# Kernel tuning notes

Measured on AMD Instinct MI355X. Metric: run time of the kernel, lower is better.

The kernel has to match this reference:

```python
import jax, jax.numpy as jnp
import numpy as np

K = 20          # neighbors
M = 8           # weight-bank size per layer
EPS = 1e-5      # BatchNorm eps


def _bn(x, axes):
    # training-mode BatchNorm at init (gamma=1, beta=0), biased variance like torch
    mu = x.mean(axes, keepdims=True)
    var = x.var(axes, keepdims=True)
    return (x - mu) * jax.lax.rsqrt(var + EPS)


def _gather(feat, idx):
    # feat [B,N,C], idx [B,N,K] -> neighbor features [B,N,K,C]
    return jax.vmap(lambda f, i: f[i])(feat, idx)


def _knn_idx(x):
    # x [B,C,N]; pairwise_distance = -||xi||^2 + 2 xi.xj - ||xj||^2 (neg sq dist)
    sq = jnp.sum(x * x, axis=1)                      # [B,N]
    inner = jnp.einsum('bcn,bcm->bnm', x, x)          # [B,N,N]
    pd = 2.0 * inner - sq[:, :, None] - sq[:, None, :]
    return jax.lax.top_k(pd, K)[1]                    # [B,N,K]


def _scorenet(xyz, w1, w2, b):
    # xyz [B,N,K,6]; 1x1 Conv2d == channel-last matmul; BN2d over (B,N,K)
    h = jax.nn.relu(_bn(xyz @ w1, (0, 1, 2)))         # [B,N,K,16]
    s = h @ w2 + b                                    # [B,N,K,M]
    return jax.nn.softmax(s, axis=-1) + 0.5           # softmax over m, bias=0.5


def _paconv(feat, idx, ker, score):
    # feat [B,N,C]; ker [2C, M*O]; score [B,N,K,M]
    # torch: point = concat(x,x) @ ker -> [B,N,M,O]; center = x @ ker[:C]
    # assemble_dgcnn (assign_score_withk, aggregate='sum'):
    #   out[b,n,o] = sum_{k,m} score[b,n,k,m] * (point[b, idx[b,n,k], m, o] - center[b, n, m, o])
    C = feat.shape[-1]
    k3 = ker.reshape(2 * C, M, -1)
    Wa, Wb = k3[:C], k3[C:]                           # point uses Wa+Wb (x repeated); center uses Wa
    nf = _gather(feat, idx)                           # [B,N,K,C]
    T = jnp.einsum('bnkm,bnkc->bnmc', score, nf)      # score-weighted neighbor feats
    out = jnp.einsum('bnmc,cmo->bno', T, Wa + Wb)
    out = out - jnp.einsum('bnm,bnc,cmo->bno', score.sum(2), feat, Wa)
    return jax.nn.relu(_bn(out, (0, 1)))              # BN1d over (B,N), channel-last


def setup_inputs() -> dict:
    key = jax.random.key(0)
    ks = jax.random.split(key, 18)
    B, N = 32, 1024
    dims = [(3, 64), (64, 64), (64, 128), (128, 256)]
    d = {"x": jax.random.normal(ks[0], (B, 3, N), dtype=jnp.float32)}
    for i, (ci, co) in enumerate(dims):
        scale = (2.0 / (2 * ci)) ** 0.5  # kaiming_normal over fan_in=2*ci
        d[f"mat{i+1}"] = jax.random.normal(ks[1 + i], (2 * ci, M * co), dtype=jnp.float32) * scale
        d[f"sn{i+1}_w1"] = jax.random.normal(ks[5 + i], (6, 16), dtype=jnp.float32) * 0.4
        d[f"sn{i+1}_w2"] = jax.random.normal(ks[9 + i], (16, M), dtype=jnp.float32) * 0.25
        d[f"sn{i+1}_b"] = jnp.zeros((M,), dtype=jnp.float32)
    d["conv5_w"] = jax.random.normal(ks[13], (512, 1024), dtype=jnp.float32) * 0.04
    d["lin1_w"] = jax.random.normal(ks[14], (2048, 512), dtype=jnp.float32) * 0.02
    d["lin2_w"] = jax.random.normal(ks[15], (512, 256), dtype=jnp.float32) * 0.04
    d["lin3_w"] = jax.random.normal(ks[16], (256, 40), dtype=jnp.float32) * 0.06
    d["lin3_b"] = jnp.zeros((40,), dtype=jnp.float32)
    return d


def reference(x, mat1, mat2, mat3, mat4,
              sn1_w1, sn1_w2, sn1_b, sn2_w1, sn2_w2, sn2_b,
              sn3_w1, sn3_w2, sn3_b, sn4_w1, sn4_w2, sn4_b,
              conv5_w, lin1_w, lin2_w, lin3_w, lin3_b):
    idx = _knn_idx(x)                                  # [B,N,K]
    xT = jnp.swapaxes(x, 1, 2)                         # [B,N,3]
    nx = _gather(xT, idx)                              # [B,N,K,3]
    xyz = jnp.concatenate([nx - xT[:, :, None, :], nx], axis=-1)  # [B,N,K,6]

    p1 = _paconv(xT, idx, mat1, _scorenet(xyz, sn1_w1, sn1_w2, sn1_b))  # [B,N,64]
    p2 = _paconv(p1, idx, mat2, _scorenet(xyz, sn2_w1, sn2_w2, sn2_b))  # [B,N,64]
    p3 = _paconv(p2, idx, mat3, _scorenet(xyz, sn3_w1, sn3_w2, sn3_b))  # [B,N,128]
    p4 = _paconv(p3, idx, mat4, _scorenet(xyz, sn4_w1, sn4_w2, sn4_b))  # [B,N,256]

    p = jnp.concatenate([p1, p2, p3, p4], axis=-1)     # [B,N,512]
    p = jax.nn.relu(_bn(p @ conv5_w, (0, 1)))          # [B,N,1024]
    g = jnp.concatenate([p.max(axis=1), p.mean(axis=1)], axis=-1)  # [B,2048]
    h = jax.nn.relu(_bn(g @ lin1_w, (0,)))             # [B,512] (dropout = identity)
    h = jax.nn.relu(_bn(h @ lin2_w, (0,)))             # [B,256]
    return h @ lin3_w + lin3_b                         # [B,40]
```

## Files before the change

### kernel.cpp

```cpp
#include <hip/hip_runtime.h>
#include <cstdint>
#include <cstddef>

static constexpr int Bc  = 32;
static constexpr int Nc  = 1024;
static constexpr int Kc  = 20;
static constexpr int Mc  = 8;
static constexpr int BNc = Bc * Nc;
static constexpr int BNKc = BNc * Kc;

typedef __attribute__((ext_vector_type(4))) float f32x4;
typedef _Float16 f16x8 __attribute__((ext_vector_type(8)));

__device__ inline short f2h(float v) { _Float16 h = (_Float16)v; return __builtin_bit_cast(short, h); }
__device__ inline float h2f(short s) { return (float)__builtin_bit_cast(_Float16, s); }

__global__ void zero_kernel(float* p, int n) {
  int gid = blockIdx.x * blockDim.x + threadIdx.x;
  if (gid < n) p[gid] = 0.f;
}

__global__ __launch_bounds__(256) void knn_kernel(const float* __restrict__ x,
                                                  int* __restrict__ idxout) {
  int wv = threadIdx.x >> 6;
  int bn = blockIdx.x * 4 + wv;
  int b = bn >> 10, n = bn & (Nc - 1);
  int lane = threadIdx.x & 63;
  const float* xb = x + (size_t)b * 3 * Nc;
  float cx = xb[n], cy = xb[Nc + n], cz = xb[2 * Nc + n];
  float sqc = cx * cx + cy * cy + cz * cz;
  float d[16];
#pragma unroll
  for (int j = 0; j < 16; j++) {
    int m2 = j * 64 + lane;
    float xm = xb[m2], ym = xb[Nc + m2], zm = xb[2 * Nc + m2];
    d[j] = 2.f * (cx * xm + cy * ym + cz * zm) - sqc - (xm * xm + ym * ym + zm * zm);
  }
  int* out = idxout + (size_t)bn * Kc;
  for (int kk = 0; kk < Kc; kk++) {
    float bd = d[0]; int bj = 0;
#pragma unroll
    for (int j = 1; j < 16; j++)
      if (d[j] > bd) { bd = d[j]; bj = j; }
    int bm = bj * 64 + lane;
#pragma unroll
    for (int off = 32; off; off >>= 1) {
      float od = __shfl_down(bd, off);
      int   om = __shfl_down(bm, off);
      if (od > bd || (od == bd && om < bm)) { bd = od; bm = om; }
    }
    bm = __shfl(bm, 0);
    if (lane == 0) out[kk] = bm;
    int bmj = bm >> 6;
    bool mine = (bm & 63) == lane;
#pragma unroll
    for (int j = 0; j < 16; j++)
      if (mine && j == bmj) d[j] = -3e38f;
  }
}

__global__ __launch_bounds__(256) void xt_kernel(const float* __restrict__ x,
                                                 float* __restrict__ xT) {
  int gid = blockIdx.x * blockDim.x + threadIdx.x;
  int c = gid % 3;
  int bn = gid / 3;
  int b = bn >> 10, n = bn & (Nc - 1);
  xT[gid] = x[((size_t)b * 3 + c) * Nc + n];
}

__device__ inline void xyz_at(const float* __restrict__ xT, const int* __restrict__ idx,
                              int e, float v[6]) {
  int bn = e / Kc;
  int b = bn >> 10;
  int nb = idx[e];
  const float* pc = xT + (size_t)bn * 3;
  const float* pn = xT + ((size_t)(b << 10) + nb) * 3;
#pragma unroll
  for (int c = 0; c < 3; c++) { float nv = pn[c]; v[c] = nv - pc[c]; v[3 + c] = nv; }
}

__global__ __launch_bounds__(256) void xyz_stats_kernel(const float* __restrict__ xT,
                                                        const int* __restrict__ idx,
                                                        float* __restrict__ accum) {
  __shared__ float sPart[4 * 42];
  int tid = threadIdx.x;
  int gid = blockIdx.x * 256 + tid;
  float a[42];
#pragma unroll
  for (int t = 0; t < 42; t++) a[t] = 0.f;
  for (int i = 0; i < 8; i++) {
    float v[6];
    xyz_at(xT, idx, gid + i * 81920, v);
#pragma unroll
    for (int c = 0; c < 6; c++) a[c] += v[c];
    int t = 6;
#pragma unroll
    for (int c = 0; c < 6; c++)
#pragma unroll
      for (int d = 0; d < 6; d++) a[t++] += v[c] * v[d];
  }
  int lane = tid & 63, wid = tid >> 6;
#pragma unroll
  for (int t = 0; t < 42; t++) {
    float v = a[t];
#pragma unroll
    for (int off = 32; off; off >>= 1) v += __shfl_down(v, off);
    if (lane == 0) sPart[wid * 42 + t] = v;
  }
  __syncthreads();
  if (tid < 42) {
    float s = sPart[tid] + sPart[42 + tid] + sPart[84 + tid] + sPart[126 + tid];
    atomicAdd(&accum[tid], s);
  }
}

__global__ void snstats_kernel(const float* __restrict__ accum,
                               const float* __restrict__ w1a, const float* __restrict__ w1b,
                               const float* __restrict__ w1c, const float* __restrict__ w1d,
                               float* __restrict__ snstats) {
  int t = threadIdx.x;
  int l = t >> 4, j = t & 15;
  const float* w1 = (l == 0) ? w1a : (l == 1) ? w1b : (l == 2) ? w1c : w1d;
  const float invc = 1.f / (float)BNKc;
  float wj[6];
  float mu = 0.f;
#pragma unroll
  for (int c = 0; c < 6; c++) { wj[c] = w1[c * 16 + j]; mu += accum[c] * invc * wj[c]; }
  float e2 = 0.f;
#pragma unroll
  for (int c = 0; c < 6; c++)
#pragma unroll
    for (int d = 0; d < 6; d++) e2 += wj[c] * wj[d] * (accum[6 + c * 6 + d] * invc);
  float var = e2 - mu * mu;
  snstats[t * 2] = mu;
  snstats[t * 2 + 1] = rsqrtf(var + 1e-5f);
}

__global__ __launch_bounds__(256) void score_kernel(const float* __restrict__ xT,
                                                    const int* __restrict__ idx,
                                                    const float* __restrict__ w1,
                                                    const float* __restrict__ w2,
                                                    const float* __restrict__ bias,
                                                    const float* __restrict__ snst,
                                                    float* __restrict__ score) {
  __shared__ float sW1[96], sW2[128], sB[8], sMu[16], sRs[16];
  int tid = threadIdx.x;
  if (tid < 96) sW1[tid] = w1[tid];
  else if (tid < 224) sW2[tid - 96] = w2[tid - 96];
  else if (tid < 232) sB[tid - 224] = bias[tid - 224];
  else if (tid < 248) { sMu[tid - 232] = snst[(tid - 232) * 2]; sRs[tid - 232] = snst[(tid - 232) * 2 + 1]; }
  __syncthreads();
  int e = blockIdx.x * 256 + tid;
  float v[6];
  xyz_at(xT, idx, e, v);
  float h[16];
#pragma unroll
  for (int j = 0; j < 16; j++) {
    float a = 0.f;
#pragma unroll
    for (int c = 0; c < 6; c++) a += v[c] * sW1[c * 16 + j];
    a = (a - sMu[j]) * sRs[j];
    h[j] = a > 0.f ? a : 0.f;
  }
  float s[8];
  float mx = -3e38f;
#pragma unroll
  for (int m = 0; m < 8; m++) {
    float a = sB[m];
#pragma unroll
    for (int j = 0; j < 16; j++) a += h[j] * sW2[j * 8 + m];
    s[m] = a;
    mx = fmaxf(mx, a);
  }
  float sum = 0.f;
#pragma unroll
  for (int m = 0; m < 8; m++) { s[m] = expf(s[m] - mx); sum += s[m]; }
  float inv = 1.f / sum;
#pragma unroll
  for (int m = 0; m < 8; m++) score[(size_t)e * 8 + m] = s[m] * inv + 0.5f;
}

template <int C, int Co, int MH>
__global__ __launch_bounds__(256) void paconv_kernel(
    const float* __restrict__ feat, int fstride,
    const float* __restrict__ ker,
    const float* __restrict__ score,
    const int* __restrict__ idx,
    float* __restrict__ outp, int ostride) {
  constexpr int PT = 8;
  constexpr int MS = Mc / MH;
  __shared__ float sX[PT][2 * MH * C];
  __shared__ float sSc[PT * Kc * Mc];
  __shared__ int sIdx[PT * Kc];
  __shared__ float sFc[PT][C];
  __shared__ float sSum[PT][Mc];

  int tid = threadIdx.x;
  int pbase = blockIdx.x * PT;
  int bN = pbase & ~(Nc - 1);

  for (int e = tid; e < PT * Kc; e += 256) sIdx[e] = idx[(size_t)pbase * Kc + e];
  for (int e = tid; e < PT * Kc * Mc; e += 256) sSc[e] = score[(size_t)pbase * Kc * Mc + e];
  for (int e = tid; e < PT * C; e += 256) {
    int p = e / C, c = e - p * C;
    sFc[p][c] = feat[(size_t)(pbase + p) * fstride + c];
  }
  __syncthreads();
  for (int e = tid; e < PT * Mc; e += 256) {
    int p = e >> 3, m = e & 7;
    float s = 0.f;
#pragma unroll
    for (int k = 0; k < Kc; k++) s += sSc[p * Kc * Mc + k * Mc + m];
    sSum[p][m] = s;
  }
  __syncthreads();

  constexpr int OG = Co;
  constexpr int PG = 256 / OG;
  constexpr int PPT = PT / PG;
  int o = tid % OG;
  int pg = tid / OG;
  float acc[PPT];
#pragma unroll
  for (int i = 0; i < PPT; i++) acc[i] = 0.f;

  for (int ms = 0; ms < MS; ms++) {
    int mb = ms * MH;
    for (int e = tid; e < PT * C; e += 256) {
      int p = e / C, c = e - p * C;
      float t[MH];
#pragma unroll
      for (int mm = 0; mm < MH; mm++) t[mm] = 0.f;
      const float* sc = &sSc[p * Kc * Mc + mb];
      for (int k = 0; k < Kc; k++) {
        float v = feat[(size_t)(bN + sIdx[p * Kc + k]) * fstride + c];
#pragma unroll
        for (int mm = 0; mm < MH; mm++) t[mm] += sc[k * Mc + mm] * v;
      }
      float fc = sFc[p][c];
#pragma unroll
      for (int mm = 0; mm < MH; mm++) {
        sX[p][mm * C + c] = t[mm] - sSum[p][mb + mm] * fc;
        sX[p][MH * C + mm * C + c] = t[mm];
      }
    }
    __syncthreads();
#pragma unroll
    for (int mm = 0; mm < MH; mm++) {
      int m = mb + mm;
      const float* kerm = ker + (size_t)m * Co + o;
      for (int c = 0; c < C; c++) {
        float wA = kerm[(size_t)c * (Mc * Co)];
        float wB = kerm[(size_t)(C + c) * (Mc * Co)];
        int r = mm * C + c;
#pragma unroll
        for (int i = 0; i < PPT; i++) {
          int p = pg * PPT + i;
          acc[i] += sX[p][r] * wA;
          acc[i] += sX[p][MH * C + r] * wB;
        }
      }
    }
    __syncthreads();
  }

#pragma unroll
  for (int i = 0; i < PPT; i++) {
    int p = pg * PPT + i;
    outp[(size_t)(pbase + p) * ostride + o] = acc[i];
  }
}

template <int C>
__global__ __launch_bounds__(256) void gather_kernel(
    const short* __restrict__ pb, int coff,
    const float* __restrict__ score,
    const int* __restrict__ idx,
    short* __restrict__ TU, int p0) {
  constexpr int PT = 256 / C;
  __shared__ float sSc[PT][Kc][Mc];
  __shared__ int   sIdx[PT][Kc];
  __shared__ float sSum[PT][Mc];
  int tid = threadIdx.x;
  int pbase = p0 + blockIdx.x * PT;
  int bbase = pbase & ~(Nc - 1);
  for (int e = tid; e < PT * Kc * Mc; e += 256) (&sSc[0][0][0])[e] = score[(size_t)pbase * Kc * Mc + e];
  for (int e = tid; e < PT * Kc; e += 256) (&sIdx[0][0])[e] = idx[(size_t)pbase * Kc + e];
  __syncthreads();
  if (tid < PT * Mc) {
    int p = tid >> 3, m = tid & 7;
    float s = 0.f;
#pragma unroll
    for (int k = 0; k < Kc; k++) s += sSc[p][k][m];
    sSum[p][m] = s;
  }
  __syncthreads();
  int p = tid / C, c = tid - p * C;
  float t[Mc];
#pragma unroll
  for (int m = 0; m < Mc; m++) t[m] = 0.f;
  for (int k = 0; k < Kc; k++) {
    float v = h2f(pb[(size_t)(bbase + sIdx[p][k]) * 512 + coff + c]);
#pragma unroll
    for (int m = 0; m < Mc; m++) t[m] += sSc[p][k][m] * v;
  }
  float fc = h2f(pb[(size_t)(pbase + p) * 512 + coff + c]);
  short* rowp = TU + (size_t)(pbase + p - p0) * (2 * Mc * C);
#pragma unroll
  for (int m = 0; m < Mc; m++) {
    rowp[m * C + c]          = f2h(t[m] - sSum[p][m] * fc);
    rowp[Mc * C + m * C + c] = f2h(t[m]);
  }
}

__global__ __launch_bounds__(256) void kerconv_kernel(const float* __restrict__ ker,
                                                      short* __restrict__ Bt,
                                                      int C, int Co, int total) {
  int gid = blockIdx.x * 256 + threadIdx.x;
  if (gid >= total) return;
  int RT = 2 * Mc * C;
  int o = gid / RT, r = gid - o * RT;
  int half = r / (Mc * C);
  int mc = r - half * Mc * C;
  int m = mc / C, c = mc - m * C;
  Bt[gid] = f2h(ker[(size_t)(half * C + c) * (Mc * Co) + m * Co + o]);
}

__global__ __launch_bounds__(256) void w5conv_kernel(const float* __restrict__ W,
                                                     short* __restrict__ Wt) {
  int gid = blockIdx.x * 256 + threadIdx.x;
  int o = gid >> 9, k = gid & 511;
  Wt[gid] = f2h(W[(size_t)k * 1024 + o]);
}

template <int BN, bool OUT_HALF>
__global__ __launch_bounds__(256) void gemm_kernel(
    const short* __restrict__ A,
    const short* __restrict__ Bt,
    int K,
    void* __restrict__ Cout, int ldc) {
  constexpr int BM = 128, BK = 64;
  constexpr int FN = BN / 32;
  __shared__ short sA[BM * BK];
  __shared__ short sB[BN * BK];
  int tid = threadIdx.x;
  int lane = tid & 63, wv = tid >> 6;
  int wrow = (wv & 1) * 64;
  int wcol = (wv >> 1) * (BN / 2);
  int bm0 = blockIdx.x * BM;
  int bn0 = blockIdx.y * BN;
  int r15 = lane & 15, quad = lane >> 4;
  int swz = r15 & 7;

  f32x4 acc[4][FN];
#pragma unroll
  for (int fm = 0; fm < 4; fm++)
#pragma unroll
    for (int fn = 0; fn < FN; fn++) acc[fm][fn] = (f32x4){0.f, 0.f, 0.f, 0.f};

  for (int k0 = 0; k0 < K; k0 += BK) {
#pragma unroll
    for (int i = 0; i < (BM * BK / 8) / 256; i++) {
      int cb = i * 256 + wv * 64;
      int chunk = cb + lane;
      int row = chunk >> 3, kc = (chunk & 7) ^ (row & 7);
      const short* g = A + (size_t)(bm0 + row) * K + k0 + kc * 8;
      __builtin_amdgcn_global_load_lds((const __attribute__((address_space(1))) void*)g,
                                       (__attribute__((address_space(3))) void*)&sA[cb * 8],
                                       16, 0, 0);
    }
#pragma unroll
    for (int i = 0; i < (BN * BK / 8) / 256; i++) {
      int cb = i * 256 + wv * 64;
      int chunk = cb + lane;
      int row = chunk >> 3, kc = (chunk & 7) ^ (row & 7);
      const short* g = Bt + (size_t)(bn0 + row) * K + k0 + kc * 8;
      __builtin_amdgcn_global_load_lds((const __attribute__((address_space(1))) void*)g,
                                       (__attribute__((address_space(3))) void*)&sB[cb * 8],
                                       16, 0, 0);
    }
    __syncthreads();
#pragma unroll
    for (int kk = 0; kk < BK; kk += 32) {
      f16x8 af[4], bf[FN];
      int ccol = (kk >> 3) + quad;
#pragma unroll
      for (int fm = 0; fm < 4; fm++)
        af[fm] = *(const f16x8*)&sA[(wrow + fm * 16 + r15) * BK + ((ccol ^ swz) * 8)];
#pragma unroll
      for (int fn = 0; fn < FN; fn++)
        bf[fn] = *(const f16x8*)&sB[(wcol + fn * 16 + r15) * BK + ((ccol ^ swz) * 8)];
#pragma unroll
      for (int fm = 0; fm < 4; fm++)
#pragma unroll
        for (int fn = 0; fn < FN; fn++)
          acc[fm][fn] = __builtin_amdgcn_mfma_f32_16x16x32_f16(af[fm], bf[fn], acc[fm][fn], 0, 0, 0);
    }
    __syncthreads();
  }

#pragma unroll
  for (int fn = 0; fn < FN; fn++) {
    int col = bn0 + wcol + fn * 16 + r15;
#pragma unroll
    for (int fm = 0; fm < 4; fm++) {
      int rowb = bm0 + wrow + fm * 16 + quad * 4;
#pragma unroll
      for (int r = 0; r < 4; r++) {
        float v = acc[fm][fn][r];
        if constexpr (OUT_HALF) ((short*)Cout)[(size_t)(rowb + r) * ldc + col] = f2h(v);
        else                    ((float*)Cout)[(size_t)(rowb + r) * ldc + col] = v;
      }
    }
  }
}

template <bool IS_HALF>
__global__ __launch_bounds__(256) void bnstats_kernel(const void* __restrict__ pre,
                                                      int Co,
                                                      float* __restrict__ bnslots) {
  __shared__ float sS[4][64], sQ[4][64];
  int tid = threadIdx.x;
  int c = tid & 63, tg = tid >> 6;
  int ch = blockIdx.x * 64 + c;
  int row0 = blockIdx.y * 1024 + tg * 256;
  float s = 0.f, q = 0.f;
  if constexpr (IS_HALF) {
    const short* p = (const short*)pre + (size_t)row0 * Co + ch;
#pragma unroll 4
    for (int r = 0; r < 256; r++) {
      float v = h2f(p[(size_t)r * Co]);
      s += v; q += v * v;
    }
  } else {
    const float* p = (const float*)pre + (size_t)row0 * Co + ch;
#pragma unroll 4
    for (int r = 0; r < 256; r++) {
      float v = p[(size_t)r * Co];
      s += v; q += v * v;
    }
  }
  sS[tg][c] = s; sQ[tg][c] = q;
  __syncthreads();
  if (tid < 64) {
    float ts = sS[0][tid] + sS[1][tid] + sS[2][tid] + sS[3][tid];
    float tq = sQ[0][tid] + sQ[1][tid] + sQ[2][tid] + sQ[3][tid];
    int chh = blockIdx.x * 64 + tid;
    bnslots[(chh * 32 + blockIdx.y) * 2 + 0] = ts;
    bnslots[(chh * 32 + blockIdx.y) * 2 + 1] = tq;
  }
}

__global__ void bnfinalize_kernel(const float* __restrict__ slots,
                                  float* __restrict__ bnmr, int Co) {
  int ch = blockIdx.x * blockDim.x + threadIdx.x;
  if (ch >= Co) return;
  float s = 0.f, q = 0.f;
#pragma unroll 4
  for (int i = 0; i < 32; i++) { s += slots[(ch * 32 + i) * 2]; q += slots[(ch * 32 + i) * 2 + 1]; }
  float mu = s / (float)BNc;
  float var = q / (float)BNc - mu * mu;
  bnmr[ch * 2] = mu;
  bnmr[ch * 2 + 1] = rsqrtf(var + 1e-5f);
}

__global__ __launch_bounds__(256) void bnapply_kernel(const float* __restrict__ pre,
                                                      int Co, const float* __restrict__ bnmr,
                                                      short* __restrict__ pb, int coff) {
  int gid = blockIdx.x * 256 + threadIdx.x;
  int row = gid / Co, ch = gid - row * Co;
  float mu = bnmr[ch * 2], rs = bnmr[ch * 2 + 1];
  float v = (pre[gid] - mu) * rs;
  pb[(size_t)row * 512 + coff + ch] = f2h(v > 0.f ? v : 0.f);
}

__global__ __launch_bounds__(512) void g2_kernel(const short* __restrict__ pre,
                                                 const float* __restrict__ bnmr,
                                                 float* __restrict__ g) {
  int b = blockIdx.x, nch = blockIdx.y;
  int tid = threadIdx.x;
  int ch0 = 2 * tid;
  float mu0 = bnmr[ch0 * 2],     rs0 = bnmr[ch0 * 2 + 1];
  float mu1 = bnmr[ch0 * 2 + 2], rs1 = bnmr[ch0 * 2 + 3];
  const uint32_t* p32 = (const uint32_t*)(pre + (size_t)b * 1024 * 1024 + (size_t)nch * 128 * 1024);
  float mx0 = 0.f, mx1 = 0.f, sm0 = 0.f, sm1 = 0.f;
#pragma unroll 4
  for (int n = 0; n < 128; n++) {
    uint32_t u = p32[n * 512 + tid];
    float v0 = (h2f((short)(u & 0xffff)) - mu0) * rs0;
    float v1 = (h2f((short)(u >> 16))    - mu1) * rs1;
    v0 = v0 > 0.f ? v0 : 0.f;
    v1 = v1 > 0.f ? v1 : 0.f;
    mx0 = fmaxf(mx0, v0); mx1 = fmaxf(mx1, v1);
    sm0 += v0; sm1 += v1;
  }
  int* gi = (int*)g;
  atomicMax(&gi[b * 2048 + ch0], __float_as_int(mx0));
  atomicMax(&gi[b * 2048 + ch0 + 1], __float_as_int(mx1));
  atomicAdd(&g[b * 2048 + 1024 + ch0], sm0 * (1.f / 1024.f));
  atomicAdd(&g[b * 2048 + 1024 + ch0 + 1], sm1 * (1.f / 1024.f));
}

__global__ __launch_bounds__(256) void linsplit_kernel(const float* __restrict__ A,
                                                       const float* __restrict__ W,
                                                       float* __restrict__ out,
                                                       int Kdim, int Cols, int kchunk) {
  int j = blockIdx.x * 256 + threadIdx.x;
  if (j >= Cols) return;
  int b = blockIdx.y;
  int k0 = blockIdx.z * kchunk;
  const float* a = A + (size_t)b * Kdim + k0;
  const float* w = W + (size_t)k0 * Cols + j;
  float acc = 0.f;
#pragma unroll 4
  for (int i = 0; i < kchunk; i++) acc += a[i] * w[(size_t)i * Cols];
  atomicAdd(&out[b * Cols + j], acc);
}

__global__ __launch_bounds__(256) void biasinit_kernel(const float* __restrict__ bias,
                                                       float* __restrict__ out, int Cols, int n) {
  int gid = blockIdx.x * 256 + threadIdx.x;
  if (gid < n) out[gid] = bias[gid % Cols];
}

__global__ __launch_bounds__(256) void lin_bn_kernel(float* __restrict__ X, int Cols) {
  int j = blockIdx.x * 256 + threadIdx.x;
  if (j >= Cols) return;
  float s = 0.f, q = 0.f;
#pragma unroll
  for (int b = 0; b < 32; b++) { float v = X[b * Cols + j]; s += v; q += v * v; }
  float mu = s * (1.f / 32.f);
  float var = q * (1.f / 32.f) - mu * mu;
  float rs = rsqrtf(var + 1e-5f);
#pragma unroll
  for (int b = 0; b < 32; b++) {
    float v = (X[b * Cols + j] - mu) * rs;
    X[b * Cols + j] = v > 0.f ? v : 0.f;
  }
}

extern "C" void kernel_launch(void* const* d_in, const int* in_sizes, int n_in,
                              void* d_out, int out_size, void* d_ws, size_t ws_size,
                              hipStream_t stream) {
  (void)in_sizes; (void)n_in; (void)out_size; (void)ws_size;
  const float* x      = (const float*)d_in[0];
  const float* mat1   = (const float*)d_in[1];
  const float* sn1_w1 = (const float*)d_in[2];
  const float* sn1_w2 = (const float*)d_in[3];
  const float* sn1_b  = (const float*)d_in[4];
  const float* mat2   = (const float*)d_in[5];
  const float* sn2_w1 = (const float*)d_in[6];
  const float* sn2_w2 = (const float*)d_in[7];
  const float* sn2_b  = (const float*)d_in[8];
  const float* mat3   = (const float*)d_in[9];
  const float* sn3_w1 = (const float*)d_in[10];
  const float* sn3_w2 = (const float*)d_in[11];
  const float* sn3_b  = (const float*)d_in[12];
  const float* mat4   = (const float*)d_in[13];
  const float* sn4_w1 = (const float*)d_in[14];
  const float* sn4_w2 = (const float*)d_in[15];
  const float* sn4_b  = (const float*)d_in[16];
  const float* conv5w = (const float*)d_in[17];
  const float* lin1w  = (const float*)d_in[18];
  const float* lin2w  = (const float*)d_in[19];
  const float* lin3w  = (const float*)d_in[20];
  const float* lin3b  = (const float*)d_in[21];
  float* out = (float*)d_out;

  char* ws = (char*)d_ws;
  size_t cur = 0;
  auto alloc = [&](size_t bytes) {
    size_t r = cur;
    cur += (bytes + 1023) & ~(size_t)1023;
    return r;
  };
  size_t off_idx   = alloc((size_t)BNKc * 4);
  size_t off_xT    = alloc((size_t)BNc * 3 * 4);
  size_t off_st    = alloc((size_t)157888 * 4);
  size_t off_score = alloc((size_t)BNKc * 8 * 4);
  size_t off_pre   = alloc((size_t)BNc * 256 * 4);
  size_t off_pb    = alloc((size_t)BNc * 512 * 2);
  size_t off_kb    = alloc((size_t)1048576);
  size_t off_TU    = alloc((size_t)BNc * 1024 * 2);

  int*   idx   = (int*)(ws + off_idx);
  float* xT    = (float*)(ws + off_xT);
  float* stats = (float*)(ws + off_st);
  float* score = (float*)(ws + off_score);
  float* pre   = (float*)(ws + off_pre);
  short* pb    = (short*)(ws + off_pb);
  short* kb    = (short*)(ws + off_kb);
  short* TU    = (short*)(ws + off_TU);
  short* pre5  = (short*)(ws + off_TU);

  float* xyzacc  = stats;
  float* snstats = stats + 64;
  float* bnslots = stats + 192;
  float* bnmr    = stats + 65728;
  float* g       = stats + 67776;
  float* h1      = stats + 133312;
  float* h2      = stats + 149696;

  zero_kernel<<<1, 64, 0, stream>>>(xyzacc, 64);
  knn_kernel<<<BNc / 4, 256, 0, stream>>>(x, idx);
  xt_kernel<<<BNc * 3 / 256, 256, 0, stream>>>(x, xT);
  xyz_stats_kernel<<<320, 256, 0, stream>>>(xT, idx, xyzacc);
  snstats_kernel<<<1, 64, 0, stream>>>(xyzacc, sn1_w1, sn2_w1, sn3_w1, sn4_w1, snstats);

  score_kernel<<<BNKc / 256, 256, 0, stream>>>(xT, idx, sn1_w1, sn1_w2, sn1_b, snstats + 0, score);
  paconv_kernel<3, 64, 8><<<BNc / 8, 256, 0, stream>>>(xT, 3, mat1, score, idx, pre, 64);
  bnstats_kernel<false><<<dim3(1, 32), 256, 0, stream>>>(pre, 64, bnslots);
  bnfinalize_kernel<<<1, 64, 0, stream>>>(bnslots, bnmr, 64);
  bnapply_kernel<<<BNc * 64 / 256, 256, 0, stream>>>(pre, 64, bnmr, pb, 0);

  score_kernel<<<BNKc / 256, 256, 0, stream>>>(xT, idx, sn2_w1, sn2_w2, sn2_b, snstats + 32, score);
  gather_kernel<64><<<BNc / 4, 256, 0, stream>>>(pb, 0, score, idx, TU, 0);
  kerconv_kernel<<<64 * 1024 / 256, 256, 0, stream>>>(mat2, kb, 64, 64, 64 * 1024);
  gemm_kernel<64, false><<<dim3(256, 1), 256, 0, stream>>>(TU, kb, 1024, pre, 64);
  bnstats_kernel<false><<<dim3(1, 32), 256, 0, stream>>>(pre, 64, bnslots);
  bnfinalize_kernel<<<1, 64, 0, stream>>>(bnslots, bnmr, 64);
  bnapply_kernel<<<BNc * 64 / 256, 256, 0, stream>>>(pre, 64, bnmr, pb, 64);

  score_kernel<<<BNKc / 256, 256, 0, stream>>>(xT, idx, sn3_w1, sn3_w2, sn3_b, snstats + 64, score);
  gather_kernel<64><<<BNc / 4, 256, 0, stream>>>(pb, 64, score, idx, TU, 0);
  kerconv_kernel<<<128 * 1024 / 256, 256, 0, stream>>>(mat3, kb, 64, 128, 128 * 1024);
  gemm_kernel<128, false><<<dim3(256, 1), 256, 0, stream>>>(TU, kb, 1024, pre, 128);
  bnstats_kernel<false><<<dim3(2, 32), 256, 0, stream>>>(pre, 128, bnslots);
  bnfinalize_kernel<<<1, 128, 0, stream>>>(bnslots, bnmr, 128);
  bnapply_kernel<<<BNc * 128 / 256, 256, 0, stream>>>(pre, 128, bnmr, pb, 128);

  score_kernel<<<BNKc / 256, 256, 0, stream>>>(xT, idx, sn4_w1, sn4_w2, sn4_b, snstats + 96, score);
  kerconv_kernel<<<256 * 2048 / 256, 256, 0, stream>>>(mat4, kb, 128, 256, 256 * 2048);
  for (int ch = 0; ch < 2; ch++) {
    int p0 = ch * 16384;
    gather_kernel<128><<<16384 / 2, 256, 0, stream>>>(pb, 128, score, idx, TU, p0);
    gemm_kernel<128, false><<<dim3(128, 2), 256, 0, stream>>>(TU, kb, 2048,
                                                              pre + (size_t)p0 * 256, 256);
  }
  bnstats_kernel<false><<<dim3(4, 32), 256, 0, stream>>>(pre, 256, bnslots);
  bnfinalize_kernel<<<1, 256, 0, stream>>>(bnslots, bnmr, 256);
  bnapply_kernel<<<BNc * 256 / 256, 256, 0, stream>>>(pre, 256, bnmr, pb, 256);

  w5conv_kernel<<<524288 / 256, 256, 0, stream>>>(conv5w, kb);
  gemm_kernel<128, true><<<dim3(256, 8), 256, 0, stream>>>(pb, kb, 512, pre5, 1024);
  bnstats_kernel<true><<<dim3(16, 32), 256, 0, stream>>>(pre5, 1024, bnslots);
  bnfinalize_kernel<<<4, 256, 0, stream>>>(bnslots, bnmr, 1024);

  zero_kernel<<<256, 256, 0, stream>>>(g, 65536);
  g2_kernel<<<dim3(32, 8), 512, 0, stream>>>(pre5, bnmr, g);

  zero_kernel<<<64, 256, 0, stream>>>(h1, 16384);
  linsplit_kernel<<<dim3(2, 32, 8), 256, 0, stream>>>(g, lin1w, h1, 2048, 512, 256);
  lin_bn_kernel<<<2, 256, 0, stream>>>(h1, 512);
  zero_kernel<<<32, 256, 0, stream>>>(h2, 8192);
  linsplit_kernel<<<dim3(1, 32, 4), 256, 0, stream>>>(h1, lin2w, h2, 512, 256, 128);
  lin_bn_kernel<<<1, 256, 0, stream>>>(h2, 256);
  biasinit_kernel<<<5, 256, 0, stream>>>(lin3b, out, 40, 1280);
  linsplit_kernel<<<dim3(1, 32, 2), 256, 0, stream>>>(h2, lin3w, out, 256, 40, 128);
}
```

Measured before the change: 876.0 us.

## Fuse scorenet into gather/paconv and BN statistics into GEMM epilogue

Computes the scorenet softmax scores inside the paconv and gather kernels instead of writing and re-reading a large score buffer, removing four score kernels and their global traffic. The GEMM epilogue now reduces per-column sum and sum-of-squares into per-block slots, eliminating the separate bnstats passes over the GEMM outputs. The GEMM tile height becomes a template parameter and is reduced to 64 for the PAConv layers, doubling block counts. The slot layout is widened to 512 slots per channel, and finalize loops over more slots, at the cost of a larger stats workspace and a serial per-channel reduction.

```diff
diff --git a/kernel.cpp b/kernel.cpp
--- a/kernel.cpp
+++ b/kernel.cpp
@@ -8,6 +8,7 @@
 static constexpr int Mc  = 8;
 static constexpr int BNc = Bc * Nc;
 static constexpr int BNKc = BNc * Kc;
+static constexpr int NSLOT = 512;
 
 typedef __attribute__((ext_vector_type(4))) float f32x4;
 typedef _Float16 f16x8 __attribute__((ext_vector_type(8)));
@@ -136,23 +137,14 @@
   snstats[t * 2 + 1] = rsqrtf(var + 1e-5f);
 }
 
-__global__ __launch_bounds__(256) void score_kernel(const float* __restrict__ xT,
-                                                    const int* __restrict__ idx,
-                                                    const float* __restrict__ w1,
-                                                    const float* __restrict__ w2,
-                                                    const float* __restrict__ bias,
-                                                    const float* __restrict__ snst,
-                                                    float* __restrict__ score) {
-  __shared__ float sW1[96], sW2[128], sB[8], sMu[16], sRs[16];
-  int tid = threadIdx.x;
-  if (tid < 96) sW1[tid] = w1[tid];
-  else if (tid < 224) sW2[tid - 96] = w2[tid - 96];
-  else if (tid < 232) sB[tid - 224] = bias[tid - 224];
-  else if (tid < 248) { sMu[tid - 232] = snst[(tid - 232) * 2]; sRs[tid - 232] = snst[(tid - 232) * 2 + 1]; }
-  __syncthreads();
-  int e = blockIdx.x * 256 + tid;
+__device__ inline void score_eval(const float* __restrict__ xT, int cg, int ng,
+                                  const float* sW1, const float* sW2, const float* sB,
+                                  const float* sMu, const float* sRs, float* outp) {
+  const float* pc = xT + (size_t)cg * 3;
+  const float* pn = xT + (size_t)ng * 3;
   float v[6];
-  xyz_at(xT, idx, e, v);
+#pragma unroll
+  for (int c = 0; c < 3; c++) { float nv = pn[c]; v[c] = nv - pc[c]; v[3 + c] = nv; }
   float h[16];
 #pragma unroll
   for (int j = 0; j < 16; j++) {
@@ -177,15 +169,17 @@
   for (int m = 0; m < 8; m++) { s[m] = expf(s[m] - mx); sum += s[m]; }
   float inv = 1.f / sum;
 #pragma unroll
-  for (int m = 0; m < 8; m++) score[(size_t)e * 8 + m] = s[m] * inv + 0.5f;
+  for (int m = 0; m < 8; m++) outp[m] = s[m] * inv + 0.5f;
 }
 
 template <int C, int Co, int MH>
 __global__ __launch_bounds__(256) void paconv_kernel(
     const float* __restrict__ feat, int fstride,
     const float* __restrict__ ker,
-    const float* __restrict__ score,
+    const float* __restrict__ xT,
     const int* __restrict__ idx,
+    const float* __restrict__ w1, const float* __restrict__ w2,
+    const float* __restrict__ bias, const float* __restrict__ snst,
     float* __restrict__ outp, int ostride) {
   constexpr int PT = 8;
   constexpr int MS = Mc / MH;
@@ -194,16 +188,26 @@
   __shared__ int sIdx[PT * Kc];
   __shared__ float sFc[PT][C];
   __shared__ float sSum[PT][Mc];
+  __shared__ float sW1[96], sW2[128], sB[8], sMu[16], sRs[16];
 
   int tid = threadIdx.x;
   int pbase = blockIdx.x * PT;
   int bN = pbase & ~(Nc - 1);
 
+  if (tid < 96) sW1[tid] = w1[tid];
+  else if (tid < 224) sW2[tid - 96] = w2[tid - 96];
+  else if (tid < 232) sB[tid - 224] = bias[tid - 224];
+  else if (tid < 248) { sMu[tid - 232] = snst[(tid - 232) * 2]; sRs[tid - 232] = snst[(tid - 232) * 2 + 1]; }
   for (int e = tid; e < PT * Kc; e += 256) sIdx[e] = idx[(size_t)pbase * Kc + e];
-  for (int e = tid; e < PT * Kc * Mc; e += 256) sSc[e] = score[(size_t)pbase * Kc * Mc + e];
   for (int e = tid; e < PT * C; e += 256) {
     int p = e / C, c = e - p * C;
     sFc[p][c] = feat[(size_t)(pbase + p) * fstride + c];
+  }
+  __syncthreads();
+  if (tid < PT * Kc) {
+    int p = tid / Kc, k = tid - p * Kc;
+    score_eval(xT, pbase + p, bN + sIdx[p * Kc + k], sW1, sW2, sB, sMu, sRs,
+               &sSc[p * Kc * Mc + k * Mc]);
   }
   __syncthreads();
   for (int e = tid; e < PT * Mc; e += 256) {
@@ -274,18 +278,29 @@
 template <int C>
 __global__ __launch_bounds__(256) void gather_kernel(
     const short* __restrict__ pb, int coff,
-    const float* __restrict__ score,
+    const float* __restrict__ xT,
     const int* __restrict__ idx,
+    const float* __restrict__ w1, const float* __restrict__ w2,
+    const float* __restrict__ bias, const float* __restrict__ snst,
     short* __restrict__ TU, int p0) {
   constexpr int PT = 256 / C;
   __shared__ float sSc[PT][Kc][Mc];
   __shared__ int   sIdx[PT][Kc];
   __shared__ float sSum[PT][Mc];
+  __shared__ float sW1[96], sW2[128], sB[8], sMu[16], sRs[16];
   int tid = threadIdx.x;
   int pbase = p0 + blockIdx.x * PT;
   int bbase = pbase & ~(Nc - 1);
-  for (int e = tid; e < PT * Kc * Mc; e += 256) (&sSc[0][0][0])[e] = score[(size_t)pbase * Kc * Mc + e];
+  if (tid < 96) sW1[tid] = w1[tid];
+  else if (tid < 224) sW2[tid - 96] = w2[tid - 96];
+  else if (tid < 232) sB[tid - 224] = bias[tid - 224];
+  else if (tid < 248) { sMu[tid - 232] = snst[(tid - 232) * 2]; sRs[tid - 232] = snst[(tid - 232) * 2 + 1]; }
   for (int e = tid; e < PT * Kc; e += 256) (&sIdx[0][0])[e] = idx[(size_t)pbase * Kc + e];
+  __syncthreads();
+  if (tid < PT * Kc) {
+    int p = tid / Kc, k = tid - p * Kc;
+    score_eval(xT, pbase + p, bbase + sIdx[p][k], sW1, sW2, sB, sMu, sRs, &sSc[p][k][0]);
+  }
   __syncthreads();
   if (tid < PT * Mc) {
     int p = tid >> 3, m = tid & 7;
@@ -333,28 +348,30 @@
   Wt[gid] = f2h(W[(size_t)k * 1024 + o]);
 }
 
-template <int BN, bool OUT_HALF>
+template <int BM, int BN, bool OUT_HALF>
 __global__ __launch_bounds__(256) void gemm_kernel(
     const short* __restrict__ A,
     const short* __restrict__ Bt,
     int K,
-    void* __restrict__ Cout, int ldc) {
-  constexpr int BM = 128, BK = 64;
+    void* __restrict__ Cout, int ldc,
+    float* __restrict__ bnslots, int slotbase) {
+  constexpr int BK = 64;
+  constexpr int FM = BM / 32;
   constexpr int FN = BN / 32;
   __shared__ short sA[BM * BK];
   __shared__ short sB[BN * BK];
   int tid = threadIdx.x;
   int lane = tid & 63, wv = tid >> 6;
-  int wrow = (wv & 1) * 64;
+  int wrow = (wv & 1) * (BM / 2);
   int wcol = (wv >> 1) * (BN / 2);
   int bm0 = blockIdx.x * BM;
   int bn0 = blockIdx.y * BN;
   int r15 = lane & 15, quad = lane >> 4;
   int swz = r15 & 7;
 
-  f32x4 acc[4][FN];
-#pragma unroll
-  for (int fm = 0; fm < 4; fm++)
+  f32x4 acc[FM][FN];
+#pragma unroll
+  for (int fm = 0; fm < FM; fm++)
 #pragma unroll
     for (int fn = 0; fn < FN; fn++) acc[fm][fn] = (f32x4){0.f, 0.f, 0.f, 0.f};
 
@@ -382,16 +399,16 @@
     __syncthreads();
 #pragma unroll
     for (int kk = 0; kk < BK; kk += 32) {
-      f16x8 af[4], bf[FN];
+      f16x8 af[FM], bf[FN];
       int ccol = (kk >> 3) + quad;
 #pragma unroll
-      for (int fm = 0; fm < 4; fm++)
+      for (int fm = 0; fm < FM; fm++)
         af[fm] = *(const f16x8*)&sA[(wrow + fm * 16 + r15) * BK + ((ccol ^ swz) * 8)];
 #pragma unroll
       for (int fn = 0; fn < FN; fn++)
         bf[fn] = *(const f16x8*)&sB[(wcol + fn * 16 + r15) * BK + ((ccol ^ swz) * 8)];
 #pragma unroll
-      for (int fm = 0; fm < 4; fm++)
+      for (int fm = 0; fm < FM; fm++)
 #pragma unroll
         for (int fn = 0; fn < FN; fn++)
           acc[fm][fn] = __builtin_amdgcn_mfma_f32_16x16x32_f16(af[fm], bf[fn], acc[fm][fn], 0, 0, 0);
@@ -399,19 +416,38 @@
     __syncthreads();
   }
 
+  float* sred = (float*)sA;
 #pragma unroll
   for (int fn = 0; fn < FN; fn++) {
     int col = bn0 + wcol + fn * 16 + r15;
-#pragma unroll
-    for (int fm = 0; fm < 4; fm++) {
+    float ps = 0.f, pq = 0.f;
+#pragma unroll
+    for (int fm = 0; fm < FM; fm++) {
       int rowb = bm0 + wrow + fm * 16 + quad * 4;
 #pragma unroll
       for (int r = 0; r < 4; r++) {
         float v = acc[fm][fn][r];
         if constexpr (OUT_HALF) ((short*)Cout)[(size_t)(rowb + r) * ldc + col] = f2h(v);
         else                    ((float*)Cout)[(size_t)(rowb + r) * ldc + col] = v;
+        ps += v; pq += v * v;
       }
     }
+    ps += __shfl_xor(ps, 16); ps += __shfl_xor(ps, 32);
+    pq += __shfl_xor(pq, 16); pq += __shfl_xor(pq, 32);
+    if (quad == 0) {
+      int cl = wcol + fn * 16 + r15;
+      sred[(wv & 1) * BN + cl] = ps;
+      sred[2 * BN + (wv & 1) * BN + cl] = pq;
+    }
+  }
+  __syncthreads();
+  if (tid < BN) {
+    float ps = sred[tid] + sred[BN + tid];
+    float pq = sred[2 * BN + tid] + sred[3 * BN + tid];
+    int col = bn0 + tid;
+    int slot = slotbase + blockIdx.x;
+    bnslots[((size_t)col * NSLOT + slot) * 2 + 0] = ps;
+    bnslots[((size_t)col * NSLOT + slot) * 2 + 1] = pq;
   }
 }
 
@@ -446,18 +482,20 @@
     float ts = sS[0][tid] + sS[1][tid] + sS[2][tid] + sS[3][tid];
     float tq = sQ[0][tid] + sQ[1][tid] + sQ[2][tid] + sQ[3][tid];
     int chh = blockIdx.x * 64 + tid;
-    bnslots[(chh * 32 + blockIdx.y) * 2 + 0] = ts;
-    bnslots[(chh * 32 + blockIdx.y) * 2 + 1] = tq;
+    bnslots[((size_t)chh * NSLOT + blockIdx.y) * 2 + 0] = ts;
+    bnslots[((size_t)chh * NSLOT + blockIdx.y) * 2 + 1] = tq;
   }
 }
 
 __global__ void bnfinalize_kernel(const float* __restrict__ slots,
-                                  float* __restrict__ bnmr, int Co) {
+                                  float* __restrict__ bnmr, int Co, int nslots) {
   int ch = blockIdx.x * blockDim.x + threadIdx.x;
   if (ch >= Co) return;
   float s = 0.f, q = 0.f;
-#pragma unroll 4
-  for (int i = 0; i < 32; i++) { s += slots[(ch * 32 + i) * 2]; q += slots[(ch * 32 + i) * 2 + 1]; }
+  for (int i = 0; i < nslots; i++) {
+    s += slots[((size_t)ch * NSLOT + i) * 2];
+    q += slots[((size_t)ch * NSLOT + i) * 2 + 1];
+  }
   float mu = s / (float)BNc;
   float var = q / (float)BNc - mu * mu;
   bnmr[ch * 2] = mu;
@@ -576,8 +614,7 @@
   };
   size_t off_idx   = alloc((size_t)BNKc * 4);
   size_t off_xT    = alloc((size_t)BNc * 3 * 4);
-  size_t off_st    = alloc((size_t)157888 * 4);
-  size_t off_score = alloc((size_t)BNKc * 8 * 4);
+  size_t off_st    = alloc((size_t)1200000 * 4);
   size_t off_pre   = alloc((size_t)BNc * 256 * 4);
   size_t off_pb    = alloc((size_t)BNc * 512 * 2);
   size_t off_kb    = alloc((size_t)1048576);
@@ -586,7 +623,6 @@
   int*   idx   = (int*)(ws + off_idx);
   float* xT    = (float*)(ws + off_xT);
   float* stats = (float*)(ws + off_st);
-  float* score = (float*)(ws + off_score);
   float* pre   = (float*)(ws + off_pre);
   short* pb    = (short*)(ws + off_pb);
   short* kb    = (short*)(ws + off_kb);
@@ -596,10 +632,10 @@
   float* xyzacc  = stats;
   float* snstats = stats + 64;
   float* bnslots = stats + 192;
-  float* bnmr    = stats + 65728;
-  float* g       = stats + 67776;
-  float* h1      = stats + 133312;
-  float* h2      = stats + 149696;
+  float* bnmr    = stats + 1048768;
+  float* g       = stats + 1050816;
+  float* h1      = stats + 1116352;
+  float* h2      = stats + 1132736;
 
   zero_kernel<<<1, 64, 0, stream>>>(xyzacc, 64);
   knn_kernel<<<BNc / 4, 256, 0, stream>>>(x, idx);
@@ -607,44 +643,41 @@
   xyz_stats_kernel<<<320, 256, 0, stream>>>(xT, idx, xyzacc);
   snstats_kernel<<<1, 64, 0, stream>>>(xyzacc, sn1_w1, sn2_w1, sn3_w1, sn4_w1, snstats);
 
-  score_kernel<<<BNKc / 256, 256, 0, stream>>>(xT, idx, sn1_w1, sn1_w2, sn1_b, snstats + 0, score);
-  paconv_kernel<3, 64, 8><<<BNc / 8, 256, 0, stream>>>(xT, 3, mat1, score, idx, pre, 64);
+  paconv_kernel<3, 64, 8><<<BNc / 8, 256, 0, stream>>>(
+      xT, 3, mat1, xT, idx, sn1_w1, sn1_w2, sn1_b, snstats + 0, pre, 64);
   bnstats_kernel<false><<<dim3(1, 32), 256, 0, stream>>>(pre, 64, bnslots);
-  bnfinalize_kernel<<<1, 64, 0, stream>>>(bnslots, bnmr, 64);
+  bnfinalize_kernel<<<1, 64, 0, stream>>>(bnslots, bnmr, 64, 32);
   bnapply_kernel<<<BNc * 64 / 256, 256, 0, stream>>>(pre, 64, bnmr, pb, 0);
 
-  score_kernel<<<BNKc / 256, 256, 0, stream>>>(xT, idx, sn2_w1, sn2_w2, sn2_b, snstats + 32, score);
-  gather_kernel<64><<<BNc / 4, 256, 0, stream>>>(pb, 0, score, idx, TU, 0);
+  gather_kernel<64><<<BNc / 4, 256, 0, stream>>>(pb, 0, xT, idx, sn2_w1, sn2_w2, sn2_b,
+                                                 snstats + 32, TU, 0);
   kerconv_kernel<<<64 * 1024 / 256, 256, 0, stream>>>(mat2, kb, 64, 64, 64 * 1024);
-  gemm_kernel<64, false><<<dim3(256, 1), 256, 0, stream>>>(TU, kb, 1024, pre, 64);
-  bnstats_kernel<false><<<dim3(1, 32), 256, 0, stream>>>(pre, 64, bnslots);
-  bnfinalize_kernel<<<1, 64, 0, stream>>>(bnslots, bnmr, 64);
+  gemm_kernel<64, 64, false><<<dim3(512, 1), 256, 0, stream>>>(TU, kb, 1024, pre, 64, bnslots, 0);
+  bnfinalize_kernel<<<1, 64, 0, stream>>>(bnslots, bnmr, 64, 512);
   bnapply_kernel<<<BNc * 64 / 256, 256, 0, stream>>>(pre, 64, bnmr, pb, 64);
 
-  score_kernel<<<BNKc / 256, 256, 0, stream>>>(xT, idx, sn3_w1, sn3_w2, sn3_b, snstats + 64, score);
-  gather_kernel<64><<<BNc / 4, 256, 0, stream>>>(pb, 64, score, idx, TU, 0);
+  gather_kernel<64><<<BNc / 4, 256, 0, stream>>>(pb, 64, xT, idx, sn3_w1, sn3_w2, sn3_b,
+                                                 snstats + 64, TU, 0);
   kerconv_kernel<<<128 * 1024 / 256, 256, 0, stream>>>(mat3, kb, 64, 128, 128 * 1024);
-  gemm_kernel<128, false><<<dim3(256, 1), 256, 0, stream>>>(TU, kb, 1024, pre, 128);
-  bnstats_kernel<false><<<dim3(2, 32), 256, 0, stream>>>(pre, 128, bnslots);
-  bnfinalize_kernel<<<1, 128, 0, stream>>>(bnslots, bnmr, 128);
+  gemm_kernel<64, 128, false><<<dim3(512, 1), 256, 0, stream>>>(TU, kb, 1024, pre, 128, bnslots, 0);
+  bnfinalize_kernel<<<1, 128, 0, stream>>>(bnslots, bnmr, 128, 512);
   bnapply_kernel<<<BNc * 128 / 256, 256, 0, stream>>>(pre, 128, bnmr, pb, 128);
 
-  score_kernel<<<BNKc / 256, 256, 0, stream>>>(xT, idx, sn4_w1, sn4_w2, sn4_b, snstats + 96, score);
   kerconv_kernel<<<256 * 2048 / 256, 256, 0, stream>>>(mat4, kb, 128, 256, 256 * 2048);
   for (int ch = 0; ch < 2; ch++) {
     int p0 = ch * 16384;
-    gather_kernel<128><<<16384 / 2, 256, 0, stream>>>(pb, 128, score, idx, TU, p0);
-    gemm_kernel<128, false><<<dim3(128, 2), 256, 0, stream>>>(TU, kb, 2048,
-                                                              pre + (size_t)p0 * 256, 256);
-  }
-  bnstats_kernel<false><<<dim3(4, 32), 256, 0, stream>>>(pre, 256, bnslots);
-  bnfinalize_kernel<<<1, 256, 0, stream>>>(bnslots, bnmr, 256);
+    gather_kernel<128><<<16384 / 2, 256, 0, stream>>>(pb, 128, xT, idx, sn4_w1, sn4_w2, sn4_b,
+                                                      snstats + 96, TU, p0);
+    gemm_kernel<64, 128, false><<<dim3(256, 2), 256, 0, stream>>>(TU, kb, 2048,
+                                                                  pre + (size_t)p0 * 256, 256,
+                                                                  bnslots, ch * 256);
+  }
+  bnfinalize_kernel<<<1, 256, 0, stream>>>(bnslots, bnmr, 256, 512);
   bnapply_kernel<<<BNc * 256 / 256, 256, 0, stream>>>(pre, 256, bnmr, pb, 256);
 
   w5conv_kernel<<<524288 / 256, 256, 0, stream>>>(conv5w, kb);
-  gemm_kernel<128, true><<<dim3(256, 8), 256, 0, stream>>>(pb, kb, 512, pre5, 1024);
-  bnstats_kernel<true><<<dim3(16, 32), 256, 0, stream>>>(pre5, 1024, bnslots);
-  bnfinalize_kernel<<<4, 256, 0, stream>>>(bnslots, bnmr, 1024);
+  gemm_kernel<128, 128, true><<<dim3(256, 8), 256, 0, stream>>>(pb, kb, 512, pre5, 1024, bnslots, 0);
+  bnfinalize_kernel<<<4, 256, 0, stream>>>(bnslots, bnmr, 1024, 256);
 
   zero_kernel<<<256, 256, 0, stream>>>(g, 65536);
   g2_kernel<<<dim3(32, 8), 512, 0, stream>>>(pre5, bnmr, g);
```

New measurement: 1.016 ms. 15.9% more time.
